# Kernel optimization log

Measured on AMD Instinct MI355X. Metric: run time of the kernel, lower is better.

## Reference

```python
import jax, jax.numpy as jnp
import numpy as np

B, T, V, E, H, C = 32, 512, 50000, 300, 1024, 2


def setup_inputs() -> dict:
    key = jax.random.key(0)
    ks = jax.random.split(key, 24)
    def w(k, shape):
        return jax.random.normal(k, shape, jnp.float32) * 0.05
    inp = {
        "padded_texts": jax.random.randint(ks[0], (B, T), 0, V),
        "lengths": jax.random.randint(ks[1], (B,), 1, T + 1),
        "emb": w(ks[2], (V, E)),
    }
    i = 3
    for layer, din in ((0, E), (1, 2 * H)):
        for d in ("f", "b"):
            inp[f"w_ih_l{layer}{d}"] = w(ks[i], (4 * H, din)); i += 1
            inp[f"w_hh_l{layer}{d}"] = w(ks[i], (4 * H, H)); i += 1
            inp[f"b_ih_l{layer}{d}"] = w(ks[i], (4 * H,)); i += 1
            inp[f"b_hh_l{layer}{d}"] = w(ks[i], (4 * H,)); i += 1
    inp["lin_w"] = w(ks[i], (C, 2 * H))
    inp["lin_b"] = w(ks[i + 1], (C,))
    return inp


def _reverse_padded(x, lengths):
    # Reverse each sequence within its valid length (pad tail clipped to idx 0;
    # those positions are masked out downstream anyway).
    Tt = x.shape[1]
    idx = jnp.clip(lengths[:, None] - 1 - jnp.arange(Tt)[None, :], 0)
    return jnp.take_along_axis(x, idx[:, :, None], axis=1)


def _run_dir(x, mask, W_ih, W_hh, b_ih, b_hh):
    # x: [B,T,D], mask: [B,T] bool. Returns ([B,T,H] outputs, [B,H] last hidden).
    Bb = x.shape[0]
    Hh = W_hh.shape[1]
    xp = jnp.einsum('btd,gd->btg', x, W_ih) + b_ih + b_hh  # [B,T,4H]
    def step(carry, inp):
        h, c = carry
        g_in, m = inp
        gates = g_in + h @ W_hh.T
        i, f, g, o = jnp.split(gates, 4, axis=-1)  # torch gate order i,f,g,o
        c_new = jax.nn.sigmoid(f) * c + jax.nn.sigmoid(i) * jnp.tanh(g)
        h_new = jax.nn.sigmoid(o) * jnp.tanh(c_new)
        m = m[:, None]
        h = jnp.where(m, h_new, h)
        c = jnp.where(m, c_new, c)
        return (h, c), h
    h0 = jnp.zeros((Bb, Hh), x.dtype)
    (hT, _), outs = jax.lax.scan(step, (h0, h0), (xp.swapaxes(0, 1), mask.T))
    return outs.swapaxes(0, 1), hT


def _bilstm_layer(x, lengths, mask, pf, pb):
    out_f, h_f = _run_dir(x, mask, *pf)
    xr = _reverse_padded(x, lengths)
    out_br, h_b = _run_dir(xr, mask, *pb)
    out_b = _reverse_padded(out_br, lengths)
    return jnp.concatenate([out_f, out_b], -1), h_f, h_b


def reference(padded_texts, lengths, emb,
              w_ih_l0f, w_hh_l0f, b_ih_l0f, b_hh_l0f,
              w_ih_l0b, w_hh_l0b, b_ih_l0b, b_hh_l0b,
              w_ih_l1f, w_hh_l1f, b_ih_l1f, b_hh_l1f,
              w_ih_l1b, w_hh_l1b, b_ih_l1b, b_hh_l1b,
              lin_w, lin_b):
    x = emb[padded_texts]  # [B,T,E]
    mask = jnp.arange(x.shape[1])[None, :] < lengths[:, None]
    x1, _, _ = _bilstm_layer(x, lengths, mask,
                             (w_ih_l0f, w_hh_l0f, b_ih_l0f, b_hh_l0f),
                             (w_ih_l0b, w_hh_l0b, b_ih_l0b, b_hh_l0b))
    _, h2f, h2b = _bilstm_layer(x1, lengths, mask,
                                (w_ih_l1f, w_hh_l1f, b_ih_l1f, b_hh_l1f),
                                (w_ih_l1b, w_hh_l1b, b_ih_l1b, b_hh_l1b))
    # torch: hn[-1] = layer-2 backward, hn[-2] = layer-2 forward;
    # source concatenates (hn[-1], hn[-2]) -> (backward, forward).
    concat = jnp.concatenate([h2b, h2f], axis=1)  # [B,2H]
    return concat @ lin_w.T + lin_b  # [B,2]
```

## Files before the change

### kernel.cpp

```cpp
#include <hip/hip_runtime.h>
#include <hip/hip_bf16.h>
#include <math.h>

typedef __bf16 bf16_8 __attribute__((ext_vector_type(8)));
typedef float  f32x4  __attribute__((ext_vector_type(4)));

#define B_   32
#define T_   512
#define H_   1024
#define G_   4096
#define E_   300
#define EP_  320
#define CT_  128
#define NCH  4

constexpr size_t OFF_HBUF  = 0;
constexpr size_t OFF_FLAGS = 524288;
constexpr size_t SZ_ZERO   = OFF_FLAGS + 131072;
constexpr size_t OFF_CBUF  = SZ_ZERO;
constexpr size_t OFF_H2F   = OFF_CBUF + 262144;
constexpr size_t OFF_H2B   = OFF_H2F + 65536;
constexpr size_t OFF_W0F   = OFF_H2B + 65536;
constexpr size_t OFF_W0B   = OFF_W0F + 2621440;
constexpr size_t OFF_W1F   = OFF_W0B + 2621440;
constexpr size_t OFF_W1B   = OFF_W1F + 16777216;
constexpr size_t OFF_EMB   = OFF_W1B + 16777216;
constexpr size_t OFF_OUTF  = OFF_EMB + 32000000;
constexpr size_t OFF_OUTB  = OFF_OUTF + 33554432;
constexpr size_t OFF_XPF   = OFF_OUTB + 33554432;
constexpr size_t OFF_XPB   = OFF_XPF + 33554432;
constexpr size_t WS_NEED   = OFF_XPB + 33554432;

#define WSTR 1032
constexpr int LDS_W  = 0;
constexpr int LDS_H  = 32 * WSTR * 2;
constexpr int LDS_G  = LDS_H + 32 * WSTR * 2;
constexpr int LDS_C  = LDS_G + 32 * 36 * 4;
constexpr int LDS_L  = LDS_C + 32 * 8 * 4;
constexpr int SMEM_REC = LDS_L + 128;

__device__ __forceinline__ float sigf(float x) { return 1.f / (1.f + __expf(-x)); }

__device__ __forceinline__ bf16_8 cvt8(f32x4 lo, f32x4 hi) {
    bf16_8 v;
    #pragma unroll
    for (int e = 0; e < 4; ++e) { v[e] = (__bf16)lo[e]; v[4 + e] = (__bf16)hi[e]; }
    return v;
}

__global__ void pad_w0(const float* __restrict__ wf, const float* __restrict__ wb,
                       __bf16* __restrict__ of, __bf16* __restrict__ ob) {
    int r = blockIdx.x, dir = blockIdx.y, k = threadIdx.x;
    const float* s = dir ? wb : wf;
    __bf16* d = (dir ? ob : of) + (size_t)r * EP_;
    d[k] = (k < E_) ? (__bf16)s[(size_t)r * E_ + k] : (__bf16)0.f;
}

__global__ void cvt_w1(const float* __restrict__ wf, const float* __restrict__ wb,
                       __bf16* __restrict__ of, __bf16* __restrict__ ob) {
    int n = blockIdx.x;
    const float* s = (blockIdx.y ? wb : wf) + (size_t)n * 2048;
    __bf16* d = (blockIdx.y ? ob : of) + (size_t)n * 2048;
    for (int k = threadIdx.x; k < 2048; k += 256) d[k] = (__bf16)s[k];
}

__global__ void cvt_emb(const float* __restrict__ emb, __bf16* __restrict__ embp) {
    int v = blockIdx.x, k = threadIdx.x;
    embp[(size_t)v * EP_ + k] = (k < E_) ? (__bf16)emb[(size_t)v * E_ + k] : (__bf16)0.f;
}

__global__ __launch_bounds__(256) void gemm_l0c(
    const int* __restrict__ texts, const int* __restrict__ lens,
    const __bf16* __restrict__ embp, const __bf16* __restrict__ W,
    const float* __restrict__ bih, const float* __restrict__ bhh,
    __bf16* __restrict__ D, int dir, int t0) {
    constexpr int LDT = 40;
    __shared__ __bf16 As[128 * LDT];
    __shared__ __bf16 Bs[128 * LDT];
    int m0 = (blockIdx.x >> 5) * 128, n0 = (blockIdx.x & 31) * 128;
    int tid = threadIdx.x;
    int rr = tid >> 2, c8 = (tid & 3) * 8;
    const __bf16* pA[2]; const __bf16* pB[2];
    #pragma unroll
    for (int s = 0; s < 2; ++s) {
        int row = m0 + rr + s * 64;
        int b = row >> 7, t = t0 + (row & 127);
        int tt = t;
        if (dir) { int L = lens[b]; tt = L - 1 - t; if (tt < 0) tt = 0; }
        pA[s] = embp + (size_t)texts[b * T_ + tt] * EP_;
        pB[s] = W + (size_t)(n0 + rr + s * 64) * EP_;
    }
    int lane = tid & 63, wid = tid >> 6;
    int wm = (wid >> 1) * 64, wn = (wid & 1) * 64;
    int row16 = lane & 15, quad = lane >> 4;
    bf16_8 apf[2], bpf[2];
    #pragma unroll
    for (int s = 0; s < 2; ++s) {
        apf[s] = *(const bf16_8*)(pA[s] + c8);
        bpf[s] = *(const bf16_8*)(pB[s] + c8);
    }
    f32x4 acc[4][4] = {};
    for (int k0 = 0; k0 < EP_; k0 += 32) {
        #pragma unroll
        for (int s = 0; s < 2; ++s) {
            *(bf16_8*)&As[(rr + s * 64) * LDT + c8] = apf[s];
            *(bf16_8*)&Bs[(rr + s * 64) * LDT + c8] = bpf[s];
        }
        __syncthreads();
        if (k0 + 32 < EP_) {
            int k8 = k0 + 32 + c8;
            #pragma unroll
            for (int s = 0; s < 2; ++s) {
                apf[s] = *(const bf16_8*)(pA[s] + k8);
                bpf[s] = *(const bf16_8*)(pB[s] + k8);
            }
        }
        bf16_8 a[4], b[4];
        #pragma unroll
        for (int i = 0; i < 4; ++i) a[i] = *(const bf16_8*)&As[(wm + i * 16 + row16) * LDT + quad * 8];
        #pragma unroll
        for (int j = 0; j < 4; ++j) b[j] = *(const bf16_8*)&Bs[(wn + j * 16 + row16) * LDT + quad * 8];
        #pragma unroll
        for (int i = 0; i < 4; ++i)
            #pragma unroll
            for (int j = 0; j < 4; ++j)
                acc[i][j] = __builtin_amdgcn_mfma_f32_16x16x32_bf16(a[i], b[j], acc[i][j], 0, 0, 0);
        __syncthreads();
    }
    #pragma unroll
    for (int j = 0; j < 4; ++j) {
        int col = n0 + wn + j * 16 + row16;
        float bias = bih[col] + bhh[col];
        #pragma unroll
        for (int i = 0; i < 4; ++i) {
            int rowb = m0 + wm + i * 16 + quad * 4;
            #pragma unroll
            for (int r = 0; r < 4; ++r)
                D[(size_t)(rowb + r) * G_ + col] = (__bf16)(acc[i][j][r] + bias);
        }
    }
}

__global__ __launch_bounds__(256) void gemm_l1c(
    const __bf16* __restrict__ outf, const __bf16* __restrict__ outbr,
    const int* __restrict__ lens, const __bf16* __restrict__ W,
    const float* __restrict__ bih, const float* __restrict__ bhh,
    __bf16* __restrict__ D, int dir, int t0) {
    constexpr int LDT = 40;
    __shared__ __bf16 As[128 * LDT];
    __shared__ __bf16 Bs[128 * LDT];
    int m0 = (blockIdx.x >> 5) * 128, n0 = (blockIdx.x & 31) * 128;
    int tid = threadIdx.x;
    int rr = tid >> 2, c8 = (tid & 3) * 8;
    const __bf16* pLo[2]; const __bf16* pHi[2]; const __bf16* pB[2];
    #pragma unroll
    for (int s = 0; s < 2; ++s) {
        int row = m0 + rr + s * 64;
        int b = row >> 7, t = t0 + (row & 127);
        int L = lens[b];
        int rev = L - 1 - t; if (rev < 0) rev = 0;
        int tf = dir ? rev : t;
        int tb = dir ? t : rev;
        pLo[s] = outf  + ((size_t)b * T_ + tf) * H_;
        pHi[s] = outbr + ((size_t)b * T_ + tb) * H_;
        pB[s]  = W + (size_t)(n0 + rr + s * 64) * (2 * H_);
    }
    int lane = tid & 63, wid = tid >> 6;
    int wm = (wid >> 1) * 64, wn = (wid & 1) * 64;
    int row16 = lane & 15, quad = lane >> 4;
    bf16_8 apf[2], bpf[2];
    #pragma unroll
    for (int s = 0; s < 2; ++s) {
        apf[s] = *(const bf16_8*)(pLo[s] + c8);
        bpf[s] = *(const bf16_8*)(pB[s] + c8);
    }
    f32x4 acc[4][4] = {};
    for (int k0 = 0; k0 < 2 * H_; k0 += 32) {
        #pragma unroll
        for (int s = 0; s < 2; ++s) {
            *(bf16_8*)&As[(rr + s * 64) * LDT + c8] = apf[s];
            *(bf16_8*)&Bs[(rr + s * 64) * LDT + c8] = bpf[s];
        }
        __syncthreads();
        if (k0 + 32 < 2 * H_) {
            int k8 = k0 + 32 + c8;
            #pragma unroll
            for (int s = 0; s < 2; ++s) {
                const __bf16* src = (k8 < H_) ? pLo[s] + k8 : pHi[s] + (k8 - H_);
                apf[s] = *(const bf16_8*)src;
                bpf[s] = *(const bf16_8*)&pB[s][k8];
            }
        }
        bf16_8 a[4], b[4];
        #pragma unroll
        for (int i = 0; i < 4; ++i) a[i] = *(const bf16_8*)&As[(wm + i * 16 + row16) * LDT + quad * 8];
        #pragma unroll
        for (int j = 0; j < 4; ++j) b[j] = *(const bf16_8*)&Bs[(wn + j * 16 + row16) * LDT + quad * 8];
        #pragma unroll
        for (int i = 0; i < 4; ++i)
            #pragma unroll
            for (int j = 0; j < 4; ++j)
                acc[i][j] = __builtin_amdgcn_mfma_f32_16x16x32_bf16(a[i], b[j], acc[i][j], 0, 0, 0);
        __syncthreads();
    }
    #pragma unroll
    for (int j = 0; j < 4; ++j) {
        int col = n0 + wn + j * 16 + row16;
        float bias = bih[col] + bhh[col];
        #pragma unroll
        for (int i = 0; i < 4; ++i) {
            int rowb = m0 + wm + i * 16 + quad * 4;
            #pragma unroll
            for (int r = 0; r < 4; ++r)
                D[(size_t)(rowb + r) * G_ + col] = (__bf16)(acc[i][j][r] + bias);
        }
    }
}

__global__ __launch_bounds__(256) void lstm_rec(
    const __bf16* __restrict__ xp_f, const __bf16* __restrict__ xp_b,
    const float* __restrict__ whh_f, const float* __restrict__ whh_b,
    const int* __restrict__ lens,
    __bf16* __restrict__ hbuf,
    float* __restrict__ cbuf,
    __bf16* __restrict__ out_f, __bf16* __restrict__ out_b,
    unsigned* __restrict__ flags,
    int t0, int seq) {
    extern __shared__ char smem[];
    __bf16* Wl = (__bf16*)(smem + LDS_W);
    __bf16* Hl = (__bf16*)(smem + LDS_H);
    float*  Gl = (float*)(smem + LDS_G);
    float*  Cl = (float*)(smem + LDS_C);
    int*    Ll = (int*)(smem + LDS_L);

    int blk = blockIdx.x;
    int dir = blk >> 7;
    int myb = blk & 127;
    int j0  = myb * 8;
    int tid = threadIdx.x;
    const __bf16* xp  = dir ? xp_b : xp_f;
    const float*  whh = dir ? whh_b : whh_f;
    __bf16* outp = dir ? out_b : out_f;
    unsigned* myflags = flags + dir * 128 * 32;

    int em = tid >> 3, eu = tid & 7;
    for (int i = tid; i < 32 * 128; i += 256) {
        int n = i >> 7, k8 = (i & 127) * 8;
        int grow = (n >> 3) * H_ + j0 + (n & 7);
        f32x4 lo = *(const f32x4*)&whh[(size_t)grow * H_ + k8];
        f32x4 hi = *(const f32x4*)&whh[(size_t)grow * H_ + k8 + 4];
        *(bf16_8*)&Wl[n * WSTR + k8] = cvt8(lo, hi);
    }
    if (tid < 32) Ll[tid] = lens[tid];
    Cl[tid] = (t0 == 0) ? 0.f : cbuf[dir * (B_ * H_) + em * H_ + j0 + eu];
    __syncthreads();

    int lane = tid & 63, wid = tid >> 6;
    int row16 = lane & 15, quad = lane >> 4;
    int m0 = (wid >> 1) * 16, n0 = (wid & 1) * 16;
    int tend = t0 + CT_;

    for (int t = t0; t < tend; ++t) {
        size_t xbase = ((size_t)em * CT_ + (t - t0)) * G_ + j0 + eu;
        __bf16 xg0 = xp[xbase];
        __bf16 xg1 = xp[xbase + H_];
        __bf16 xg2 = xp[xbase + 2 * H_];
        __bf16 xg3 = xp[xbase + 3 * H_];
        const __bf16* hs = hbuf + (size_t)((t & 1) * 2 + dir) * (B_ * H_);
        f32x4 hreg[16];
        #pragma unroll
        for (int s = 0; s < 16; ++s) {
            int idx = tid + s * 256;
            int mm = idx >> 7, k8 = (idx & 127) * 8;
            const __bf16* p = hs + mm * H_ + k8;
            asm volatile("global_load_dwordx4 %0, %1, off sc0 sc1"
                         : "=v"(hreg[s]) : "v"(p));
        }
        asm volatile("s_waitcnt vmcnt(0)" ::: "memory");
        __builtin_amdgcn_sched_barrier(0);
        #pragma unroll
        for (int s = 0; s < 16; ++s) {
            int idx = tid + s * 256;
            int mm = idx >> 7, k8 = (idx & 127) * 8;
            *(bf16_8*)&Hl[mm * WSTR + k8] = *(bf16_8*)&hreg[s];
        }
        __syncthreads();
        f32x4 acc0 = {0.f, 0.f, 0.f, 0.f}, acc1 = {0.f, 0.f, 0.f, 0.f};
        #pragma unroll
        for (int kc = 0; kc < 32; kc += 2) {
            bf16_8 a0 = *(const bf16_8*)&Hl[(m0 + row16) * WSTR + kc * 32 + quad * 8];
            bf16_8 b0 = *(const bf16_8*)&Wl[(n0 + row16) * WSTR + kc * 32 + quad * 8];
            acc0 = __builtin_amdgcn_mfma_f32_16x16x32_bf16(a0, b0, acc0, 0, 0, 0);
            bf16_8 a1 = *(const bf16_8*)&Hl[(m0 + row16) * WSTR + (kc + 1) * 32 + quad * 8];
            bf16_8 b1 = *(const bf16_8*)&Wl[(n0 + row16) * WSTR + (kc + 1) * 32 + quad * 8];
            acc1 = __builtin_amdgcn_mfma_f32_16x16x32_bf16(a1, b1, acc1, 0, 0, 0);
        }
        #pragma unroll
        for (int r = 0; r < 4; ++r)
            Gl[(m0 + quad * 4 + r) * 36 + n0 + row16] = acc0[r] + acc1[r];
        __syncthreads();
        {
            float pi = Gl[em * 36 + eu]      + (float)xg0;
            float pf = Gl[em * 36 + 8 + eu]  + (float)xg1;
            float pg = Gl[em * 36 + 16 + eu] + (float)xg2;
            float po = Gl[em * 36 + 24 + eu] + (float)xg3;
            float co = Cl[tid];
            float cn = sigf(pf) * co + sigf(pi) * tanhf(pg);
            float hn = sigf(po) * tanhf(cn);
            __bf16 heff;
            if (t < Ll[em]) { Cl[tid] = cn; heff = (__bf16)hn; }
            else            { heff = Hl[em * WSTR + j0 + eu]; }
            {
                __bf16* hp = &hbuf[(size_t)(((t + 1) & 1) * 2 + dir) * (B_ * H_) + em * H_ + j0 + eu];
                unsigned hv = (unsigned)*(unsigned short*)&heff;
                asm volatile("global_store_short %0, %1, off sc0 sc1"
                             :: "v"(hp), "v"(hv) : "memory");
            }
            if (seq)              outp[((size_t)em * T_ + t) * H_ + j0 + eu] = heff;
            else if (t == T_ - 1) outp[(size_t)em * H_ + j0 + eu] = heff;
        }
        if (t + 1 < tend) {
            __syncthreads();
            if (tid == 0)
                __hip_atomic_store(&myflags[myb * 32], (unsigned)(t + 1),
                                   __ATOMIC_RELAXED, __HIP_MEMORY_SCOPE_AGENT);
            if (tid < 128) {
                while (__hip_atomic_load(&myflags[tid * 32], __ATOMIC_RELAXED,
                                         __HIP_MEMORY_SCOPE_AGENT) < (unsigned)(t + 1))
                    __builtin_amdgcn_s_sleep(1);
            }
            __syncthreads();
        }
    }
    cbuf[dir * (B_ * H_) + em * H_ + j0 + eu] = Cl[tid];
}

__global__ void final_linear(const __bf16* __restrict__ h2f, const __bf16* __restrict__ h2b,
                             const float* __restrict__ lin_w, const float* __restrict__ lin_b,
                             float* __restrict__ out) {
    __shared__ float red[4];
    int b = blockIdx.x >> 1, c = blockIdx.x & 1;
    int tid = threadIdx.x;
    const __bf16* hb = h2b + (size_t)b * H_;
    const __bf16* hf = h2f + (size_t)b * H_;
    const float* w = lin_w + (size_t)c * (2 * H_);
    float s = 0.f;
    for (int j = tid; j < H_; j += 256)
        s += (float)hb[j] * w[j] + (float)hf[j] * w[H_ + j];
    for (int off = 32; off; off >>= 1) s += __shfl_down(s, off, 64);
    if ((tid & 63) == 0) red[tid >> 6] = s;
    __syncthreads();
    if (tid == 0)
        out[b * 2 + c] = red[0] + red[1] + red[2] + red[3] + lin_b[c];
}

extern "C" void kernel_launch(void* const* d_in, const int* in_sizes, int n_in,
                              void* d_out, int out_size, void* d_ws, size_t ws_size,
                              hipStream_t stream) {
    const int*   texts = (const int*)d_in[0];
    const int*   lens  = (const int*)d_in[1];
    const float* emb   = (const float*)d_in[2];
    const float* wih0f = (const float*)d_in[3];
    const float* whh0f = (const float*)d_in[4];
    const float* bih0f = (const float*)d_in[5];
    const float* bhh0f = (const float*)d_in[6];
    const float* wih0b = (const float*)d_in[7];
    const float* whh0b = (const float*)d_in[8];
    const float* bih0b = (const float*)d_in[9];
    const float* bhh0b = (const float*)d_in[10];
    const float* wih1f = (const float*)d_in[11];
    const float* whh1f = (const float*)d_in[12];
    const float* bih1f = (const float*)d_in[13];
    const float* bhh1f = (const float*)d_in[14];
    const float* wih1b = (const float*)d_in[15];
    const float* whh1b = (const float*)d_in[16];
    const float* bih1b = (const float*)d_in[17];
    const float* bhh1b = (const float*)d_in[18];
    const float* linw  = (const float*)d_in[19];
    const float* linb  = (const float*)d_in[20];

    char* ws = (char*)d_ws;
    __bf16*   hbuf  = (__bf16*)(ws + OFF_HBUF);
    unsigned* flags = (unsigned*)(ws + OFF_FLAGS);
    float*    cbuf  = (float*)(ws + OFF_CBUF);
    __bf16*   h2f   = (__bf16*)(ws + OFF_H2F);
    __bf16*   h2b   = (__bf16*)(ws + OFF_H2B);
    __bf16*   w0f   = (__bf16*)(ws + OFF_W0F);
    __bf16*   w0b   = (__bf16*)(ws + OFF_W0B);
    __bf16*   w1f   = (__bf16*)(ws + OFF_W1F);
    __bf16*   w1b   = (__bf16*)(ws + OFF_W1B);
    __bf16*   embp  = (__bf16*)(ws + OFF_EMB);
    __bf16*   outf  = (__bf16*)(ws + OFF_OUTF);
    __bf16*   outbr = (__bf16*)(ws + OFF_OUTB);
    __bf16*   xpf   = (__bf16*)(ws + OFF_XPF);
    __bf16*   xpb   = (__bf16*)(ws + OFF_XPB);

    if (ws_size < WS_NEED) return;

    hipMemsetAsync(ws, 0, SZ_ZERO, stream);
    hipFuncSetAttribute((const void*)lstm_rec, hipFuncAttributeMaxDynamicSharedMemorySize, SMEM_REC);

    pad_w0 <<<dim3(G_, 2), 320, 0, stream>>>(wih0f, wih0b, w0f, w0b);
    cvt_w1 <<<dim3(G_, 2), 256, 0, stream>>>(wih1f, wih1b, w1f, w1b);
    cvt_emb<<<50000, 320, 0, stream>>>(emb, embp);

    __bf16* hb0 = hbuf;
    __bf16* hb1 = hbuf + 131072;
    unsigned* fl0 = flags;
    unsigned* fl1 = flags + 2 * 128 * 32;

    for (int c = 0; c < NCH; ++c) {
        int t0 = c * CT_;
        gemm_l0c<<<1024, 256, 0, stream>>>(texts, lens, embp, w0f, bih0f, bhh0f, xpf, 0, t0);
        gemm_l0c<<<1024, 256, 0, stream>>>(texts, lens, embp, w0b, bih0b, bhh0b, xpb, 1, t0);
        lstm_rec<<<256, 256, SMEM_REC, stream>>>(xpf, xpb, whh0f, whh0b, lens,
                                                 hb0, cbuf, outf, outbr, fl0, t0, 1);
    }
    for (int c = 0; c < NCH; ++c) {
        int t0 = c * CT_;
        gemm_l1c<<<1024, 256, 0, stream>>>(outf, outbr, lens, w1f, bih1f, bhh1f, xpf, 0, t0);
        gemm_l1c<<<1024, 256, 0, stream>>>(outf, outbr, lens, w1b, bih1b, bhh1b, xpb, 1, t0);
        lstm_rec<<<256, 256, SMEM_REC, stream>>>(xpf, xpb, whh1f, whh1b, lens,
                                                 hb1, cbuf, h2f, h2b, fl1, t0, 0);
    }
    final_linear<<<B_ * 2, 256, 0, stream>>>(h2f, h2b, linw, linb, (float*)d_out);
}
```

Measured before the change: 5.699 ms.

## Replace block-level flag barrier with per-wave flag posts and per-thread dependency polling

Each of the four waves in a block now posts its own step counter into a packed 4-word flag slot right after its own h store completes. Every thread then polls the four flags of the one source block whose h slice it is about to load, before loading. This drops the two block-wide syncthreads and the single-thread-post / 128-thread-poll barrier at the end of each step, so blocks only wait for the data they actually read. The h-load mapping is changed so each thread reads columns from a single source block. In exchange, all 256 threads poll flags without sleeping, which adds memory traffic. Correctness depends on the sc0 sc1 store and load ordering being sufficient without explicit fences.

```diff
diff --git a/kernel.cpp b/kernel.cpp
--- a/kernel.cpp
+++ b/kernel.cpp
@@ -4,6 +4,7 @@
 
 typedef __bf16 bf16_8 __attribute__((ext_vector_type(8)));
 typedef float  f32x4  __attribute__((ext_vector_type(4)));
+typedef unsigned u32x4 __attribute__((ext_vector_type(4)));
 
 #define B_   32
 #define T_   512
@@ -241,9 +242,14 @@
     const __bf16* xp  = dir ? xp_b : xp_f;
     const float*  whh = dir ? whh_b : whh_f;
     __bf16* outp = dir ? out_b : out_f;
-    unsigned* myflags = flags + dir * 128 * 32;
+    unsigned* myflags = flags + dir * 128 * 4;
 
     int em = tid >> 3, eu = tid & 7;
+    int src  = tid & 127;
+    int half = tid >> 7;
+    const unsigned* pollp = myflags + src * 4;
+    unsigned* postp = myflags + myb * 4 + (tid >> 6);
+
     for (int i = tid; i < 32 * 128; i += 256) {
         int n = i >> 7, k8 = (i & 127) * 8;
         int grow = (n >> 3) * H_ + j0 + (n & 7);
@@ -266,24 +272,28 @@
         __bf16 xg1 = xp[xbase + H_];
         __bf16 xg2 = xp[xbase + 2 * H_];
         __bf16 xg3 = xp[xbase + 3 * H_];
+        if (t > 0) {
+            while (true) {
+                u32x4 f;
+                asm volatile("global_load_dwordx4 %0, %1, off sc0 sc1"
+                             : "=v"(f) : "v"(pollp));
+                asm volatile("s_waitcnt vmcnt(0)" ::: "memory");
+                if ((int)f[0] >= t && (int)f[1] >= t && (int)f[2] >= t && (int)f[3] >= t) break;
+            }
+        }
         const __bf16* hs = hbuf + (size_t)((t & 1) * 2 + dir) * (B_ * H_);
         f32x4 hreg[16];
         #pragma unroll
         for (int s = 0; s < 16; ++s) {
-            int idx = tid + s * 256;
-            int mm = idx >> 7, k8 = (idx & 127) * 8;
-            const __bf16* p = hs + mm * H_ + k8;
+            const __bf16* p = hs + (half + 2 * s) * H_ + src * 8;
             asm volatile("global_load_dwordx4 %0, %1, off sc0 sc1"
                          : "=v"(hreg[s]) : "v"(p));
         }
         asm volatile("s_waitcnt vmcnt(0)" ::: "memory");
         __builtin_amdgcn_sched_barrier(0);
         #pragma unroll
-        for (int s = 0; s < 16; ++s) {
-            int idx = tid + s * 256;
-            int mm = idx >> 7, k8 = (idx & 127) * 8;
-            *(bf16_8*)&Hl[mm * WSTR + k8] = *(bf16_8*)&hreg[s];
-        }
+        for (int s = 0; s < 16; ++s)
+            *(bf16_8*)&Hl[(half + 2 * s) * WSTR + src * 8] = *(bf16_8*)&hreg[s];
         __syncthreads();
         f32x4 acc0 = {0.f, 0.f, 0.f, 0.f}, acc1 = {0.f, 0.f, 0.f, 0.f};
         #pragma unroll
@@ -319,18 +329,13 @@
             if (seq)              outp[((size_t)em * T_ + t) * H_ + j0 + eu] = heff;
             else if (t == T_ - 1) outp[(size_t)em * H_ + j0 + eu] = heff;
         }
-        if (t + 1 < tend) {
-            __syncthreads();
-            if (tid == 0)
-                __hip_atomic_store(&myflags[myb * 32], (unsigned)(t + 1),
-                                   __ATOMIC_RELAXED, __HIP_MEMORY_SCOPE_AGENT);
-            if (tid < 128) {
-                while (__hip_atomic_load(&myflags[tid * 32], __ATOMIC_RELAXED,
-                                         __HIP_MEMORY_SCOPE_AGENT) < (unsigned)(t + 1))
-                    __builtin_amdgcn_s_sleep(1);
-            }
-            __syncthreads();
-        }
+        asm volatile("s_waitcnt vmcnt(0)" ::: "memory");
+        if ((tid & 63) == 0) {
+            unsigned fv = (unsigned)(t + 1);
+            asm volatile("global_store_dword %0, %1, off sc0 sc1"
+                         :: "v"(postp), "v"(fv) : "memory");
+        }
+        __syncthreads();
     }
     cbuf[dir * (B_ * H_) + em * H_ + j0 + eu] = Cl[tid];
 }
@@ -407,7 +412,7 @@
     __bf16* hb0 = hbuf;
     __bf16* hb1 = hbuf + 131072;
     unsigned* fl0 = flags;
-    unsigned* fl1 = flags + 2 * 128 * 32;
+    unsigned* fl1 = flags + 2 * 128 * 4;
 
     for (int c = 0; c < NCH; ++c) {
         int t0 = c * CT_;
```

Result: slower. 7.624 ms (+33.8%).
